# Kernel tuning notes

Hardware: AMD Instinct MI355X
Metric: run time of the kernel (lower is better)

## Reference

```python
import jax, jax.numpy as jnp
import numpy as np

VOCAB, EMBED, HID = 282, 7, 51
B, T = 256, 1024

def _lstm_cell(x, h, c, w_ih, w_hh, b):
    # gates: [B, 4*HID] ; PyTorch LSTMCell gate order: i, f, g, o
    gates = x @ w_ih.T + h @ w_hh.T + b
    i, f, g, o = jnp.split(gates, 4, axis=-1)
    c_new = jax.nn.sigmoid(f) * c + jax.nn.sigmoid(i) * jnp.tanh(g)
    h_new = jax.nn.sigmoid(o) * jnp.tanh(c_new)
    return h_new, c_new

def setup_inputs() -> dict:
    key = jax.random.key(0)
    ks = jax.random.split(key, 12)
    s = lambda fan: 1.0 / np.sqrt(fan)
    u = lambda k, shp, b: jax.random.uniform(k, shp, jnp.float32, -b, b)
    return {
        "input": jax.random.randint(ks[0], (B, T), 0, VOCAB),
        "future": 0,
        "embed": jax.random.normal(ks[1], (VOCAB, EMBED), jnp.float32),
        "w_ih1": u(ks[2], (4 * HID, EMBED), s(HID)),
        "w_hh1": u(ks[3], (4 * HID, HID), s(HID)),
        "b1":    u(ks[4], (4 * HID,), s(HID)) + u(ks[5], (4 * HID,), s(HID)),
        "w_ih2": u(ks[6], (4 * HID, HID), s(HID)),
        "w_hh2": u(ks[7], (4 * HID, HID), s(HID)),
        "b2":    u(ks[8], (4 * HID,), s(HID)) + u(ks[9], (4 * HID,), s(HID)),
        "w_lin": u(ks[10], (VOCAB, HID), s(HID)),
        "b_lin": u(ks[11], (VOCAB,), s(HID)),
    }

def reference(input, future, embed, w_ih1, w_hh1, b1, w_ih2, w_hh2, b2, w_lin, b_lin):
    bsz = input.shape[0]
    xs = embed[input].transpose(1, 0, 2)  # [T, B, EMBED]
    z = jnp.zeros((bsz, HID), jnp.float32)

    def step(carry, x_t):
        h1, c1, h2, c2 = carry
        h1, c1 = _lstm_cell(x_t, h1, c1, w_ih1, w_hh1, b1)
        h2, c2 = _lstm_cell(h1, h2, c2, w_ih2, w_hh2, b2)
        out = h2 @ w_lin.T + b_lin  # [B, VOCAB]
        return (h1, c1, h2, c2), out

    carry, outs = jax.lax.scan(step, (z, z, z, z), xs)

    def fstep(carry_out, _):
        (h1, c1, h2, c2), out = carry_out
        tok = jnp.argmax(out, axis=1)
        x_t = embed[tok]
        h1, c1 = _lstm_cell(x_t, h1, c1, w_ih1, w_hh1, b1)
        h2, c2 = _lstm_cell(h1, h2, c2, w_ih2, w_hh2, b2)
        out = h2 @ w_lin.T + b_lin
        return ((h1, c1, h2, c2), out), out

    if future > 0:
        _, fouts = jax.lax.scan(fstep, (carry, outs[-1]), None, length=future)
        outs = jnp.concatenate([outs, fouts], axis=0)

    return outs.transpose(1, 0, 2)  # [B, T(+future), VOCAB]
```

## Files before the change

kernel.cpp:

```cpp
#include <hip/hip_runtime.h>

#define HID    51
#define G4     204
#define EMB    7
#define VOCAB  282
#define TT     1024
#define BB     256

__device__ __forceinline__ float sigf(float x) {
    return 1.0f / (1.0f + __expf(-x));
}
__device__ __forceinline__ float tanh_fast(float x) {
    return 1.0f - 2.0f / (__expf(2.0f * x) + 1.0f);
}

__global__ void eproj_kernel(const float* __restrict__ embed,
                             const float* __restrict__ w_ih1,
                             const float* __restrict__ b1,
                             float* __restrict__ eproj) {
    int idx = blockIdx.x * blockDim.x + threadIdx.x;
    if (idx >= VOCAB * G4) return;
    int v = idx / G4;
    int j = idx - v * G4;
    float acc = b1[j];
    #pragma unroll
    for (int e = 0; e < EMB; e++)
        acc += embed[v * EMB + e] * w_ih1[j * EMB + e];
    eproj[idx] = acc;
}

__launch_bounds__(256, 1)
__global__ void lstm_kernel(const int* __restrict__ input,
                            const float* __restrict__ eproj,
                            const float* __restrict__ w_hh1,
                            const float* __restrict__ w_ih2,
                            const float* __restrict__ w_hh2,
                            const float* __restrict__ b2,
                            float* __restrict__ out) {
    __shared__ float h1s[52];
    __shared__ float h2s[52];
    __shared__ float g1s[G4];
    __shared__ float g2s[G4];
    __shared__ int   toks[TT];

    const int j = threadIdx.x;
    const int b = blockIdx.x;

    for (int i = j; i < TT; i += 256) toks[i] = input[b * TT + i];
    if (j < 52) { h1s[j] = 0.0f; h2s[j] = 0.0f; }

    float wh1[HID], wi2[HID], wh2[HID];
    float b2j = 0.0f;
    if (j < G4) {
        #pragma unroll
        for (int k = 0; k < HID; k++) {
            wh1[k] = w_hh1[j * HID + k];
            wi2[k] = w_ih2[j * HID + k];
            wh2[k] = w_hh2[j * HID + k];
        }
        b2j = b2[j];
    }
    float c1 = 0.0f, c2 = 0.0f;
    __syncthreads();

    float gpref = (j < G4) ? eproj[toks[0] * G4 + j] : 0.0f;

    for (int t = 0; t < TT; t++) {
        float g1in = gpref;
        if (j < G4 && (t + 1) < TT)
            gpref = eproj[toks[t + 1] * G4 + j];

        if (j < G4) {
            float acc = g1in;
            #pragma unroll
            for (int k = 0; k < HID; k++) acc += wh1[k] * h1s[k];
            g1s[j] = acc;
        }
        __syncthreads();

        if (j < HID) {
            float ig = sigf(g1s[j]);
            float fg = sigf(g1s[j + HID]);
            float gg = tanh_fast(g1s[j + 2 * HID]);
            float og = sigf(g1s[j + 3 * HID]);
            c1 = fg * c1 + ig * gg;
            h1s[j] = og * tanh_fast(c1);
        }
        __syncthreads();

        if (j < G4) {
            float acc = b2j;
            #pragma unroll
            for (int k = 0; k < HID; k++) acc += wi2[k] * h1s[k];
            #pragma unroll
            for (int k = 0; k < HID; k++) acc += wh2[k] * h2s[k];
            g2s[j] = acc;
        }
        __syncthreads();

        if (j < HID) {
            float ig = sigf(g2s[j]);
            float fg = sigf(g2s[j + HID]);
            float gg = tanh_fast(g2s[j + 2 * HID]);
            float og = sigf(g2s[j + 3 * HID]);
            c2 = fg * c2 + ig * gg;
            float h2 = og * tanh_fast(c2);
            h2s[j] = h2;
            out[((size_t)b * TT + t) * VOCAB + j] = h2;
        }
        __syncthreads();
    }
}

#define CB     320
#define CROWS  32

__launch_bounds__(CB, 1)
__global__ void logits_kernel(const float* __restrict__ w_lin,
                              const float* __restrict__ b_lin,
                              float* __restrict__ out) {
    __shared__ float wl[VOCAB * HID];
    __shared__ float bl[VOCAB];
    __shared__ float h2r[CROWS][52];

    const int tid = threadIdx.x;
    const size_t r0 = (size_t)blockIdx.x * CROWS;

    for (int i = tid; i < VOCAB * HID; i += CB) wl[i] = w_lin[i];
    for (int i = tid; i < VOCAB; i += CB)       bl[i] = b_lin[i];
    for (int i = tid; i < CROWS * HID; i += CB) {
        int row = i / HID, k = i - row * HID;
        h2r[row][k] = out[(r0 + row) * VOCAB + k];
    }
    __syncthreads();

    if (tid < VOCAB) {
        float wr[HID];
        #pragma unroll
        for (int k = 0; k < HID; k++) wr[k] = wl[tid * HID + k];
        float bv = bl[tid];
        for (int row = 0; row < CROWS; row++) {
            float acc = bv;
            #pragma unroll
            for (int k = 0; k < HID; k++) acc += wr[k] * h2r[row][k];
            out[(r0 + row) * VOCAB + tid] = acc;
        }
    }
}

extern "C" void kernel_launch(void* const* d_in, const int* in_sizes, int n_in,
                              void* d_out, int out_size, void* d_ws, size_t ws_size,
                              hipStream_t stream) {
    const int*   input = (const int*)  d_in[0];
    const float* embed = (const float*)d_in[2];
    const float* w_ih1 = (const float*)d_in[3];
    const float* w_hh1 = (const float*)d_in[4];
    const float* b1    = (const float*)d_in[5];
    const float* w_ih2 = (const float*)d_in[6];
    const float* w_hh2 = (const float*)d_in[7];
    const float* b2    = (const float*)d_in[8];
    const float* w_lin = (const float*)d_in[9];
    const float* b_lin = (const float*)d_in[10];
    float* out   = (float*)d_out;
    float* eproj = (float*)d_ws;

    const int n1 = VOCAB * G4;
    eproj_kernel<<<(n1 + 255) / 256, 256, 0, stream>>>(embed, w_ih1, b1, eproj);
    lstm_kernel<<<BB, 256, 0, stream>>>(input, eproj, w_hh1, w_ih2, w_hh2, b2, out);
    logits_kernel<<<(BB * TT) / CROWS, CB, 0, stream>>>(w_lin, b_lin, out);
}
```

Measured before the change: 1.970 ms.

## Pipeline LSTM layers across warp halves with shuffle-based gate exchange

The LSTM kernel now runs 512 threads, with layer 1 in the first half and layer 2 one timestep behind in the second half. Double-buffered h vectors let both layers advance on a single barrier per step instead of four. Each hidden unit's four gates sit on adjacent lanes, so the gates are exchanged with __shfl_xor rather than a shared-memory round trip. Outputs are batched eight steps at a time, and the dot products use float4 shared loads with split accumulators (also in the logits kernel). The cost is one extra pipeline step, heavier register use under launch_bounds(512,2), and more complex lane-mapping logic.

Result: faster. 1.622 ms (-17.6%).

```diff
diff --git a/kernel.cpp b/kernel.cpp
--- a/kernel.cpp
+++ b/kernel.cpp
@@ -7,9 +7,6 @@
 #define TT     1024
 #define BB     256
 
-__device__ __forceinline__ float sigf(float x) {
-    return 1.0f / (1.0f + __expf(-x));
-}
 __device__ __forceinline__ float tanh_fast(float x) {
     return 1.0f - 2.0f / (__expf(2.0f * x) + 1.0f);
 }
@@ -29,7 +26,7 @@
     eproj[idx] = acc;
 }
 
-__launch_bounds__(256, 1)
+__launch_bounds__(512, 2)
 __global__ void lstm_kernel(const int* __restrict__ input,
                             const float* __restrict__ eproj,
                             const float* __restrict__ w_hh1,
@@ -37,76 +34,129 @@
                             const float* __restrict__ w_hh2,
                             const float* __restrict__ b2,
                             float* __restrict__ out) {
-    __shared__ float h1s[52];
-    __shared__ float h2s[52];
-    __shared__ float g1s[G4];
-    __shared__ float g2s[G4];
-    __shared__ int   toks[TT];
-
-    const int j = threadIdx.x;
-    const int b = blockIdx.x;
-
-    for (int i = j; i < TT; i += 256) toks[i] = input[b * TT + i];
-    if (j < 52) { h1s[j] = 0.0f; h2s[j] = 0.0f; }
-
-    float wh1[HID], wi2[HID], wh2[HID];
-    float b2j = 0.0f;
-    if (j < G4) {
+    __shared__ __align__(16) float h1b[2][52];
+    __shared__ __align__(16) float h2b[2][52];
+    __shared__ int toks[TT];
+
+    const int tid = threadIdx.x;
+    const int b   = blockIdx.x;
+
+    for (int i = tid; i < TT; i += 512) toks[i] = input[b * TT + i];
+    if (tid < 52) {
+        h1b[0][tid] = 0.f; h1b[1][tid] = 0.f;
+        h2b[0][tid] = 0.f; h2b[1][tid] = 0.f;
+    }
+
+    const bool isL2 = (tid >= 256);
+    const int  lt   = isL2 ? (tid - 256) : tid;
+    const int  w    = lt >> 6;
+    const int  l    = lt & 63;
+    const int  jj   = l >> 2;
+    const int  q    = l & 3;
+    const int  ne   = (w < 3) ? 13 : 12;
+    const bool al   = (jj < ne);
+    const int  j    = 13 * w + jj;
+    const int  gs   = al ? (q * 51 + j) : 0;
+
+    __syncthreads();
+
+    float wA[51], wB[51];
+    float b2g = 0.f;
+    if (!isL2) {
         #pragma unroll
-        for (int k = 0; k < HID; k++) {
-            wh1[k] = w_hh1[j * HID + k];
-            wi2[k] = w_ih2[j * HID + k];
-            wh2[k] = w_hh2[j * HID + k];
-        }
-        b2j = b2[j];
-    }
-    float c1 = 0.0f, c2 = 0.0f;
-    __syncthreads();
-
-    float gpref = (j < G4) ? eproj[toks[0] * G4 + j] : 0.0f;
-
-    for (int t = 0; t < TT; t++) {
-        float g1in = gpref;
-        if (j < G4 && (t + 1) < TT)
-            gpref = eproj[toks[t + 1] * G4 + j];
-
-        if (j < G4) {
-            float acc = g1in;
+        for (int k = 0; k < 51; k++) { wA[k] = w_hh1[gs * 51 + k]; wB[k] = 0.f; }
+    } else {
+        #pragma unroll
+        for (int k = 0; k < 51; k++) { wA[k] = w_ih2[gs * 51 + k]; wB[k] = w_hh2[gs * 51 + k]; }
+        b2g = b2[gs];
+    }
+
+    float c = 0.f, hb0 = 0.f, hb1 = 0.f;
+    float ep_cur = 0.f;
+    if (!isL2) ep_cur = eproj[toks[0] * G4 + gs];
+
+    for (int s = 0; s <= TT; ++s) {
+        const int rp = (s + 1) & 1;
+        const int wp = s & 1;
+
+        float x;
+        if (!isL2) {
+            const int sn = (s + 1 < TT) ? (s + 1) : 0;
+            const float ep_nxt = eproj[toks[sn] * G4 + gs];
+
+            float a0 = 0.f, a1 = 0.f, a2 = 0.f, a3 = 0.f;
+            const float4* hp = (const float4*)h1b[rp];
             #pragma unroll
-            for (int k = 0; k < HID; k++) acc += wh1[k] * h1s[k];
-            g1s[j] = acc;
-        }
-        __syncthreads();
-
-        if (j < HID) {
-            float ig = sigf(g1s[j]);
-            float fg = sigf(g1s[j + HID]);
-            float gg = tanh_fast(g1s[j + 2 * HID]);
-            float og = sigf(g1s[j + 3 * HID]);
-            c1 = fg * c1 + ig * gg;
-            h1s[j] = og * tanh_fast(c1);
-        }
-        __syncthreads();
-
-        if (j < G4) {
-            float acc = b2j;
+            for (int i = 0; i < 13; i++) {
+                float4 hv = hp[i];
+                const int k = 4 * i;
+                a0 += wA[k] * hv.x;
+                if (k + 1 < 51) a1 += wA[k + 1] * hv.y;
+                if (k + 2 < 51) a2 += wA[k + 2] * hv.z;
+                if (k + 3 < 51) a3 += wA[k + 3] * hv.w;
+            }
+            x = (a0 + a1) + (a2 + a3) + ep_cur;
+
+            const float As = (q == 2) ? 2.f : 1.f;
+            const float Bs = (q == 2) ? -1.f : 0.f;
+            const float act = As / (1.f + __expf(-As * x)) + Bs;
+            const float v0 = act;
+            const float v1 = __shfl_xor(act, 1);
+            const float v2 = __shfl_xor(act, 2);
+            const float v3 = __shfl_xor(v2, 1);
+            const float t0 = (q & 1) ? v1 : v0, t1 = (q & 1) ? v0 : v1;
+            const float t2 = (q & 1) ? v3 : v2, t3 = (q & 1) ? v2 : v3;
+            const float I = (q & 2) ? t2 : t0, F = (q & 2) ? t3 : t1;
+            const float G = (q & 2) ? t0 : t2, O = (q & 2) ? t1 : t3;
+            const float cn = F * c + I * G;
+            const float hn = O * tanh_fast(cn);
+            if (s < TT) {
+                c = cn;
+                if (q == 0 && al) h1b[wp][j] = hn;
+            }
+            ep_cur = ep_nxt;
+        } else {
+            const int t = s - 1;
+            float a0 = 0.f, a1 = 0.f, a2 = 0.f, a3 = 0.f;
+            const float4* hp1 = (const float4*)h1b[rp];
+            const float4* hp2 = (const float4*)h2b[wp];
             #pragma unroll
-            for (int k = 0; k < HID; k++) acc += wi2[k] * h1s[k];
-            #pragma unroll
-            for (int k = 0; k < HID; k++) acc += wh2[k] * h2s[k];
-            g2s[j] = acc;
-        }
-        __syncthreads();
-
-        if (j < HID) {
-            float ig = sigf(g2s[j]);
-            float fg = sigf(g2s[j + HID]);
-            float gg = tanh_fast(g2s[j + 2 * HID]);
-            float og = sigf(g2s[j + 3 * HID]);
-            c2 = fg * c2 + ig * gg;
-            float h2 = og * tanh_fast(c2);
-            h2s[j] = h2;
-            out[((size_t)b * TT + t) * VOCAB + j] = h2;
+            for (int i = 0; i < 13; i++) {
+                float4 ha = hp1[i];
+                float4 hb = hp2[i];
+                const int k = 4 * i;
+                a0 += wA[k] * ha.x;       a2 += wB[k] * hb.x;
+                if (k + 1 < 51) { a1 += wA[k + 1] * ha.y; a3 += wB[k + 1] * hb.y; }
+                if (k + 2 < 51) { a0 += wA[k + 2] * ha.z; a2 += wB[k + 2] * hb.z; }
+                if (k + 3 < 51) { a1 += wA[k + 3] * ha.w; a3 += wB[k + 3] * hb.w; }
+            }
+            x = (a0 + a1) + (a2 + a3) + b2g;
+
+            const float As = (q == 2) ? 2.f : 1.f;
+            const float Bs = (q == 2) ? -1.f : 0.f;
+            const float act = As / (1.f + __expf(-As * x)) + Bs;
+            const float v0 = act;
+            const float v1 = __shfl_xor(act, 1);
+            const float v2 = __shfl_xor(act, 2);
+            const float v3 = __shfl_xor(v2, 1);
+            const float t0 = (q & 1) ? v1 : v0, t1 = (q & 1) ? v0 : v1;
+            const float t2 = (q & 1) ? v3 : v2, t3 = (q & 1) ? v2 : v3;
+            const float I = (q & 2) ? t2 : t0, F = (q & 2) ? t3 : t1;
+            const float G = (q & 2) ? t0 : t2, O = (q & 2) ? t1 : t3;
+            const float cn = F * c + I * G;
+            const float hn = O * tanh_fast(cn);
+            if (t >= 0) {
+                c = cn;
+                if (q == 0 && al) h2b[t & 1][j] = hn;
+                const int ph = t & 7;
+                if (ph == 2 * q)     hb0 = hn;
+                if (ph == 2 * q + 1) hb1 = hn;
+                if (ph == 7 && al) {
+                    const size_t base = (size_t)b * TT + (t & ~7);
+                    out[(base + 2 * q)     * VOCAB + j] = hb0;
+                    out[(base + 2 * q + 1) * VOCAB + j] = hb1;
+                }
+            }
         }
         __syncthreads();
     }
@@ -121,7 +171,7 @@
                               float* __restrict__ out) {
     __shared__ float wl[VOCAB * HID];
     __shared__ float bl[VOCAB];
-    __shared__ float h2r[CROWS][52];
+    __shared__ __align__(16) float h2r[CROWS][52];
 
     const int tid = threadIdx.x;
     const size_t r0 = (size_t)blockIdx.x * CROWS;
@@ -132,18 +182,29 @@
         int row = i / HID, k = i - row * HID;
         h2r[row][k] = out[(r0 + row) * VOCAB + k];
     }
+    if (tid < CROWS) h2r[tid][51] = 0.f;
     __syncthreads();
 
     if (tid < VOCAB) {
-        float wr[HID];
+        float wr[51];
         #pragma unroll
-        for (int k = 0; k < HID; k++) wr[k] = wl[tid * HID + k];
-        float bv = bl[tid];
-        for (int row = 0; row < CROWS; row++) {
-            float acc = bv;
+        for (int k = 0; k < 51; k++) wr[k] = wl[tid * HID + k];
+        const float bv = bl[tid];
+        for (int row = 0; row < CROWS; row += 2) {
+            float a0 = 0.f, a1 = 0.f, c0 = 0.f, c1 = 0.f;
+            const float4* hp0 = (const float4*)h2r[row];
+            const float4* hp1 = (const float4*)h2r[row + 1];
             #pragma unroll
-            for (int k = 0; k < HID; k++) acc += wr[k] * h2r[row][k];
-            out[(r0 + row) * VOCAB + tid] = acc;
+            for (int i = 0; i < 13; i++) {
+                float4 h0 = hp0[i], h1 = hp1[i];
+                const int k = 4 * i;
+                a0 += wr[k] * h0.x;  c0 += wr[k] * h1.x;
+                if (k + 1 < 51) { a1 += wr[k + 1] * h0.y; c1 += wr[k + 1] * h1.y; }
+                if (k + 2 < 51) { a0 += wr[k + 2] * h0.z; c0 += wr[k + 2] * h1.z; }
+                if (k + 3 < 51) { a1 += wr[k + 3] * h0.w; c1 += wr[k + 3] * h1.w; }
+            }
+            out[(r0 + row)     * VOCAB + tid] = a0 + a1 + bv;
+            out[(r0 + row + 1) * VOCAB + tid] = c0 + c1 + bv;
         }
     }
 }
@@ -166,6 +227,6 @@
 
     const int n1 = VOCAB * G4;
     eproj_kernel<<<(n1 + 255) / 256, 256, 0, stream>>>(embed, w_ih1, b1, eproj);
-    lstm_kernel<<<BB, 256, 0, stream>>>(input, eproj, w_hh1, w_ih2, w_hh2, b2, out);
+    lstm_kernel<<<BB, 512, 0, stream>>>(input, eproj, w_hh1, w_ih2, w_hh2, b2, out);
     logits_kernel<<<(BB * TT) / CROWS, CB, 0, stream>>>(w_lin, b_lin, out);
 }
```
